# Optimization experiments

Measured on AMD Instinct MI355X. Metric: run time of the kernel, lower is better.

Reference implementation:

```python
import jax, jax.numpy as jnp
import numpy as np
from jax import lax

B, C, H, W = 4, 64, 256, 256
T, Q = 16, 0.2
C2 = 2 * C


def conv2d(x, w, b, pad):
    y = lax.conv_general_dilated(x, w, (1, 1), [(pad, pad), (pad, pad)],
                                 dimension_numbers=('NCHW', 'OIHW', 'NCHW'))
    return y + b[None, :, None, None]


def setup_inputs() -> dict:
    key = jax.random.key(0)
    ks = jax.random.split(key, 10)
    x = jax.random.normal(ks[0], (B, C, H, W), dtype=jnp.float32)
    lms = jax.random.normal(ks[1], (B, 4, H, W), dtype=jnp.float32)
    # params (kaiming-ish scale)
    W_conv = jax.random.normal(ks[2], (C2, C, 3, 3), dtype=jnp.float32) * (1.0 / np.sqrt(C * 9))
    b_conv = jnp.zeros((C2,), dtype=jnp.float32)
    W_out = jax.random.normal(ks[3], (4, C2), dtype=jnp.float32) * (1.0 / np.sqrt(C2))  # 1x1 conv as matrix
    b_out = jnp.zeros((4,), dtype=jnp.float32)
    W_aue = jax.random.normal(ks[4], (4, C2, 3, 3), dtype=jnp.float32) * (1.0 / np.sqrt(C2 * 9))
    b_aue = jnp.zeros((4,), dtype=jnp.float32)
    # T Bernoulli(1-q) channel masks, fixed for reproducibility  [T, 2C]
    masks = jax.random.bernoulli(ks[5], 1.0 - Q, (T, C2)).astype(jnp.float32)
    return {"x": x, "lms": lms, "W_conv": W_conv, "b_conv": b_conv,
            "W_out": W_out, "b_out": b_out, "W_aue": W_aue, "b_aue": b_aue,
            "masks": masks}


def reference(x, lms, W_conv, b_conv, W_out, b_out, W_aue, b_aue, masks):
    # feature extraction: 3x3 conv C -> 2C
    h = conv2d(x, W_conv, b_conv, 1)                      # [B, 2C, H, W]
    # MC-dropout samples: out(mask_t * h) == (W_out * mask_t) @ h  (1x1 conv is linear)
    Wt = W_out[None, :, :] * masks[:, None, :]            # [T, 4, 2C]
    samples = jnp.tanh(jnp.einsum('toc,bchw->tbohw', Wt, h)
                       + b_out[None, None, :, None, None]) + lms[None]  # [T, B, 4, H, W]
    mean = jnp.mean(samples, axis=0)
    EU = jnp.var(samples, axis=0, ddof=1)                 # unbiased variance over T
    AU = jax.nn.sigmoid(conv2d(h, W_aue, b_aue, 1))       # [B, 4, H, W]
    return (AU, EU, mean)
```

## Files before the change

kernel.cpp:

```cpp
#include <hip/hip_runtime.h>

#define Bsz 4
#define Cin 64
#define C2c 128
#define Hh 256
#define Ww 256
#define Tt 16
#define HW (Hh*Ww)
#define PLANE (Bsz*4*HW)

typedef __attribute__((ext_vector_type(8))) short bf16x8;
typedef __attribute__((ext_vector_type(4))) float f32x4;

#define XT_OFF  0
#define WBF_OFF 33554432
#define WTB_OFF 33701888
#define AUB_OFF 33718272

#define XP 76
#define HP 132

__device__ __forceinline__ unsigned short f2bf(float f) {
  union { float f; unsigned u; } cv; cv.f = f;
  unsigned u = cv.u;
  unsigned r = (u + 0x7fffu + ((u >> 16) & 1u)) >> 16;
  return (unsigned short)r;
}

union U8 { uint2 u2[2]; uint4 u4; bf16x8 v; };

__global__ void prep_kernel(const float* __restrict__ W_out, const float* __restrict__ masks,
                            const float* __restrict__ Wc, const float* __restrict__ W_aue,
                            unsigned short* __restrict__ Wtb, unsigned short* __restrict__ Wbf,
                            unsigned short* __restrict__ Aub) {
  int i = blockIdx.x * 256 + threadIdx.x;
  if (i < 8192) {
    int to = i >> 7, c = i & 127;
    int t = to >> 2, o = to & 3;
    Wtb[i] = f2bf(W_out[o * C2c + c] * masks[t * C2c + c]);
  } else if (i < 8192 + 73728) {
    int idx = i - 8192;
    int j = idx & 7;
    int lane = (idx >> 3) & 63;
    int nt = (idx >> 9) & 7;
    int c = idx >> 12;
    int q = lane >> 4;
    int tap = c >> 1;
    int ic = (c & 1) * 32 + q * 8 + j;
    int n = nt * 16 + (lane & 15);
    Wbf[idx] = f2bf(Wc[((size_t)n * Cin + ic) * 9 + tap]);
  } else if (i < 8192 + 73728 + 18432) {
    int idx = i - 8192 - 73728;
    int m = idx / 1152, k = idx % 1152;
    int tap = k >> 7, c = k & 127;
    float v = (m < 4) ? W_aue[((size_t)m * C2c + c) * 9 + tap] : 0.f;
    Aub[idx] = f2bf(v);
  }
}

__global__ __launch_bounds__(256) void xt_kernel(const float* __restrict__ x,
                                                 unsigned short* __restrict__ xT) {
  __shared__ unsigned short xs[64][65];
  const int tid = threadIdx.x;
  const int x0 = blockIdx.x * 64, y = blockIdx.y, bi = blockIdx.z;
  const int tx = tid & 63, ti = tid >> 6;
  #pragma unroll
  for (int i = 0; i < 16; ++i) {
    int ic = ti * 16 + i;
    float v = x[(((size_t)bi * Cin + ic) * Hh + y) * Ww + x0 + tx];
    xs[ic][tx] = f2bf(v);
  }
  __syncthreads();
  const int icg = tid & 7, xl = tid >> 3;
  #pragma unroll
  for (int rep = 0; rep < 2; ++rep) {
    int xx = xl + 32 * rep;
    unsigned short u[8];
    #pragma unroll
    for (int k = 0; k < 8; ++k) u[k] = xs[icg * 8 + k][xx];
    *(uint4*)(xT + (((size_t)bi * Hh + y) * Ww + (x0 + xx)) * Cin + icg * 8) = *(uint4*)u;
  }
}

__global__ __launch_bounds__(256, 3) void fused_kernel(
    const unsigned short* __restrict__ xT, const unsigned short* __restrict__ Wbf,
    const unsigned short* __restrict__ Wtb, const unsigned short* __restrict__ Aub,
    const float* __restrict__ bc, const float* __restrict__ b_out,
    const float* __restrict__ b_aue, const float* __restrict__ lms,
    float* __restrict__ out) {
  __shared__ unsigned short sh[192 * HP];
  const int tid = threadIdx.x;
  const int x0 = blockIdx.x * 16, y0 = blockIdx.y * 8, bi = blockIdx.z;

  for (int g = tid; g < 12 * 20 * 8; g += 256) {
    int icg = g & 7;
    int xc = (g >> 3) % 20;
    int xr = g / 160;
    int gy = y0 - 2 + xr, gx = x0 - 2 + xc;
    uint2 lo = make_uint2(0, 0), hi = make_uint2(0, 0);
    if ((unsigned)gy < Hh && (unsigned)gx < Ww) {
      uint4 v = *(const uint4*)(xT + (((size_t)bi * Hh + gy) * Ww + gx) * Cin + icg * 8);
      lo.x = v.x; lo.y = v.y; hi.x = v.z; hi.y = v.w;
    }
    int e = (xr * 20 + xc) * XP + icg * 8;
    *(uint2*)(&sh[e]) = lo;
    *(uint2*)(&sh[e + 4]) = hi;
  }
  __syncthreads();

  const int lane = tid & 63, wv = tid >> 6;
  const int n16 = lane & 15, q = lane >> 4;

  int xbase[3];
  #pragma unroll
  for (int s = 0; s < 3; ++s) {
    int px = (wv * 3 + s) * 16 + n16;
    int pr = px / 18, pc = px % 18;
    xbase[s] = (pr * 20 + pc) * XP + q * 8;
  }

  f32x4 acc[3][8];
  #pragma unroll
  for (int s = 0; s < 3; ++s)
    #pragma unroll
    for (int mt = 0; mt < 8; ++mt) acc[s][mt] = (f32x4){0.f, 0.f, 0.f, 0.f};

  #pragma unroll
  for (int c = 0; c < 18; ++c) {
    const int tap = c >> 1, ichalf = (c & 1) * 32;
    const int dy = tap / 3, dx = tap % 3;
    const int xoff = (dy * 20 + dx) * XP + ichalf;
    bf16x8 xfr[3];
    #pragma unroll
    for (int s = 0; s < 3; ++s) {
      U8 t;
      int e = xbase[s] + xoff;
      t.u2[0] = *(const uint2*)(&sh[e]);
      t.u2[1] = *(const uint2*)(&sh[e + 4]);
      xfr[s] = t.v;
    }
    #pragma unroll
    for (int mh = 0; mh < 2; ++mh) {
      bf16x8 wfr[4];
      const unsigned short* wb = Wbf + ((size_t)(c * 8 + mh * 4) * 64 + lane) * 8;
      #pragma unroll
      for (int i4 = 0; i4 < 4; ++i4)
        wfr[i4] = ((const U8*)(wb + i4 * 512))->v;
      #pragma unroll
      for (int s = 0; s < 3; ++s)
        #pragma unroll
        for (int i4 = 0; i4 < 4; ++i4)
          acc[s][mh * 4 + i4] =
            __builtin_amdgcn_mfma_f32_16x16x32_bf16(wfr[i4], xfr[s], acc[s][mh * 4 + i4], 0, 0, 0);
    }
  }
  __syncthreads();

  #pragma unroll
  for (int s = 0; s < 3; ++s) {
    const int px = (wv * 3 + s) * 16 + n16;
    const int pr = px / 18, pc = px % 18;
    const int gy = y0 - 1 + pr, gx = x0 - 1 + pc;
    const bool valid = ((unsigned)gy < Hh) && ((unsigned)gx < Ww);
    #pragma unroll
    for (int mt = 0; mt < 8; ++mt) {
      const int oc0 = mt * 16 + q * 4;
      const float4 b4 = *(const float4*)(bc + oc0);
      ushort4 o4;
      o4.x = valid ? f2bf(acc[s][mt][0] + b4.x) : (unsigned short)0;
      o4.y = valid ? f2bf(acc[s][mt][1] + b4.y) : (unsigned short)0;
      o4.z = valid ? f2bf(acc[s][mt][2] + b4.z) : (unsigned short)0;
      o4.w = valid ? f2bf(acc[s][mt][3] + b4.w) : (unsigned short)0;
      *(ushort4*)(&sh[px * HP + oc0]) = o4;
    }
  }
  __syncthreads();

  f32x4 accG[2][4];
  f32x4 accA[2];
  #pragma unroll
  for (int nt = 0; nt < 2; ++nt) {
    accA[nt] = (f32x4){0.f, 0.f, 0.f, 0.f};
    #pragma unroll
    for (int mt = 0; mt < 4; ++mt) accG[nt][mt] = (f32x4){0.f, 0.f, 0.f, 0.f};
  }

  #pragma unroll
  for (int kc = 0; kc < 4; ++kc) {
    bf16x8 afr[4];
    #pragma unroll
    for (int mt = 0; mt < 4; ++mt)
      afr[mt] = ((const U8*)(Wtb + (size_t)(mt * 16 + n16) * C2c + kc * 32 + q * 8))->v;
    #pragma unroll
    for (int nt = 0; nt < 2; ++nt) {
      int e = (((wv * 2 + nt) + 1) * 18 + n16 + 1) * HP + kc * 32 + q * 8;
      U8 b;
      b.u2[0] = *(const uint2*)(&sh[e]);
      b.u2[1] = *(const uint2*)(&sh[e + 4]);
      #pragma unroll
      for (int mt = 0; mt < 4; ++mt)
        accG[nt][mt] = __builtin_amdgcn_mfma_f32_16x16x32_bf16(afr[mt], b.v, accG[nt][mt], 0, 0, 0);
    }
  }

  #pragma unroll
  for (int kc = 0; kc < 36; ++kc) {
    const int tap = kc >> 2, co = (kc & 3) * 32;
    const int dy = tap / 3, dx = tap % 3;
    bf16x8 afr = ((const U8*)(Aub + (size_t)n16 * 1152 + kc * 32 + q * 8))->v;
    #pragma unroll
    for (int nt = 0; nt < 2; ++nt) {
      int e = ((wv * 2 + nt + dy) * 18 + n16 + dx) * HP + co + q * 8;
      U8 b;
      b.u2[0] = *(const uint2*)(&sh[e]);
      b.u2[1] = *(const uint2*)(&sh[e + 4]);
      accA[nt] = __builtin_amdgcn_mfma_f32_16x16x32_bf16(afr, b.v, accA[nt], 0, 0, 0);
    }
  }

  const float b0 = b_out[0], b1 = b_out[1], b2 = b_out[2], b3 = b_out[3];
  const float ba = b_aue[q];
  const int px = x0 + n16;
  #pragma unroll
  for (int nt = 0; nt < 2; ++nt) {
    const int y = y0 + wv * 2 + nt;
    float th[4][4];
    #pragma unroll
    for (int mt = 0; mt < 4; ++mt) {
      #pragma unroll
      for (int r = 0; r < 4; ++r) {
        float bo = (r == 0) ? b0 : (r == 1) ? b1 : (r == 2) ? b2 : b3;
        float v = accG[nt][mt][r] + bo;
        float e = __expf(2.f * v);
        th[mt][r] = 1.f - 2.f / (e + 1.f);
      }
    }
    float mean_r[4], eu_r[4];
    #pragma unroll
    for (int r = 0; r < 4; ++r) {
      float s = th[0][r] + th[1][r] + th[2][r] + th[3][r];
      s += __shfl_xor(s, 16);
      s += __shfl_xor(s, 32);
      float m = s * (1.f / 16.f);
      float d0 = th[0][r] - m, d1 = th[1][r] - m, d2 = th[2][r] - m, d3 = th[3][r] - m;
      float vs = d0 * d0 + d1 * d1 + d2 * d2 + d3 * d3;
      vs += __shfl_xor(vs, 16);
      vs += __shfl_xor(vs, 32);
      mean_r[r] = m;
      eu_r[r] = vs * (1.f / 15.f);
    }
    float au_r[4];
    #pragma unroll
    for (int r = 0; r < 4; ++r) au_r[r] = __shfl(accA[nt][r], n16);

    float m_q  = (q == 0) ? mean_r[0] : (q == 1) ? mean_r[1] : (q == 2) ? mean_r[2] : mean_r[3];
    float eu_q = (q == 0) ? eu_r[0]   : (q == 1) ? eu_r[1]   : (q == 2) ? eu_r[2]   : eu_r[3];
    float au_q = (q == 0) ? au_r[0]   : (q == 1) ? au_r[1]   : (q == 2) ? au_r[2]   : au_r[3];
    au_q = 1.f / (1.f + __expf(-(au_q + ba)));
    size_t oidx = ((size_t)(bi * 4 + q)) * HW + (size_t)y * Ww + px;
    float lm = lms[oidx];
    out[oidx] = au_q;
    out[PLANE + oidx] = eu_q;
    out[2 * (size_t)PLANE + oidx] = m_q + lm;
  }
}

extern "C" void kernel_launch(void* const* d_in, const int* in_sizes, int n_in,
                              void* d_out, int out_size, void* d_ws, size_t ws_size,
                              hipStream_t stream) {
  const float* x      = (const float*)d_in[0];
  const float* lms    = (const float*)d_in[1];
  const float* W_conv = (const float*)d_in[2];
  const float* b_conv = (const float*)d_in[3];
  const float* W_out  = (const float*)d_in[4];
  const float* b_out  = (const float*)d_in[5];
  const float* W_aue  = (const float*)d_in[6];
  const float* b_aue  = (const float*)d_in[7];
  const float* masks  = (const float*)d_in[8];
  float* out = (float*)d_out;

  char* ws = (char*)d_ws;
  unsigned short* xT  = (unsigned short*)(ws + XT_OFF);
  unsigned short* Wbf = (unsigned short*)(ws + WBF_OFF);
  unsigned short* Wtb = (unsigned short*)(ws + WTB_OFF);
  unsigned short* Aub = (unsigned short*)(ws + AUB_OFF);

  prep_kernel<<<dim3(392), dim3(256), 0, stream>>>(W_out, masks, W_conv, W_aue, Wtb, Wbf, Aub);
  xt_kernel<<<dim3(4, 256, 4), dim3(256), 0, stream>>>(x, xT);
  fused_kernel<<<dim3(16, 32, 4), dim3(256), 0, stream>>>(xT, Wbf, Wtb, Aub, b_conv,
                                                          b_out, b_aue, lms, out);
}
```

Baseline: 224.0 us.

## Merge prep into transpose kernel, async LDS loads with swizzled layouts

Folds the weight-prep kernel into the x-transpose kernel as an extra grid slice, which removes one launch, and widens the transpose to float4 loads with packed bf16 conversion. The fused kernel now fills its input halo tile with direct global-to-LDS loads (reading a zero pad buffer for out-of-range pixels), split into two channel halves so compute on the first half can start while the second half is still arriving. The padded LDS strides are replaced by XOR-swizzled layouts that allow single 16-byte LDS reads. The kernel also raises wave priority around MFMA bursts, skips stores for unused pixel slots, and shrinks the AU weight matrix to four rows. The explicit waitcnt and barrier ordering is fragile and must exactly match the number of loads issued.

Result: faster. 216.4 us (-3.4%).

```diff
diff --git a/kernel.cpp b/kernel.cpp
--- a/kernel.cpp
+++ b/kernel.cpp
@@ -16,9 +16,12 @@
 #define WBF_OFF 33554432
 #define WTB_OFF 33701888
 #define AUB_OFF 33718272
-
-#define XP 76
-#define HP 132
+#define ZP_OFF  33727488
+
+#define N_WTB 8192
+#define N_WBF 73728
+#define N_AUB 4608
+#define N_ZP  64
 
 __device__ __forceinline__ unsigned short f2bf(float f) {
   union { float f; unsigned u; } cv; cv.f = f;
@@ -27,96 +30,113 @@
   return (unsigned short)r;
 }
 
+__device__ __forceinline__ unsigned cvtpk(float a, float b) {
+  unsigned r;
+  asm("v_cvt_pk_bf16_f32 %0, %1, %2" : "=v"(r) : "v"(a), "v"(b));
+  return r;
+}
+
 union U8 { uint2 u2[2]; uint4 u4; bf16x8 v; };
 
-__global__ void prep_kernel(const float* __restrict__ W_out, const float* __restrict__ masks,
-                            const float* __restrict__ Wc, const float* __restrict__ W_aue,
-                            unsigned short* __restrict__ Wtb, unsigned short* __restrict__ Wbf,
-                            unsigned short* __restrict__ Aub) {
-  int i = blockIdx.x * 256 + threadIdx.x;
-  if (i < 8192) {
-    int to = i >> 7, c = i & 127;
-    int t = to >> 2, o = to & 3;
-    Wtb[i] = f2bf(W_out[o * C2c + c] * masks[t * C2c + c]);
-  } else if (i < 8192 + 73728) {
-    int idx = i - 8192;
-    int j = idx & 7;
-    int lane = (idx >> 3) & 63;
-    int nt = (idx >> 9) & 7;
-    int c = idx >> 12;
-    int q = lane >> 4;
-    int tap = c >> 1;
-    int ic = (c & 1) * 32 + q * 8 + j;
-    int n = nt * 16 + (lane & 15);
-    Wbf[idx] = f2bf(Wc[((size_t)n * Cin + ic) * 9 + tap]);
-  } else if (i < 8192 + 73728 + 18432) {
-    int idx = i - 8192 - 73728;
-    int m = idx / 1152, k = idx % 1152;
-    int tap = k >> 7, c = k & 127;
-    float v = (m < 4) ? W_aue[((size_t)m * C2c + c) * 9 + tap] : 0.f;
-    Aub[idx] = f2bf(v);
-  }
-}
-
-__global__ __launch_bounds__(256) void xt_kernel(const float* __restrict__ x,
-                                                 unsigned short* __restrict__ xT) {
-  __shared__ unsigned short xs[64][65];
+#define GLOAD16(g, l) __builtin_amdgcn_global_load_lds( \
+    (const __attribute__((address_space(1))) unsigned int*)(g), \
+    (__attribute__((address_space(3))) unsigned int*)(l), 16, 0, 0)
+
+__global__ __launch_bounds__(256) void xtp_kernel(
+    const float* __restrict__ x, const float* __restrict__ W_out,
+    const float* __restrict__ masks, const float* __restrict__ Wc,
+    const float* __restrict__ W_aue,
+    unsigned short* __restrict__ xT, unsigned short* __restrict__ Wtb,
+    unsigned short* __restrict__ Wbf, unsigned short* __restrict__ Aub,
+    unsigned short* __restrict__ Zp) {
+  __shared__ unsigned short xs[64 * 132];
   const int tid = threadIdx.x;
-  const int x0 = blockIdx.x * 64, y = blockIdx.y, bi = blockIdx.z;
-  const int tx = tid & 63, ti = tid >> 6;
-  #pragma unroll
-  for (int i = 0; i < 16; ++i) {
-    int ic = ti * 16 + i;
-    float v = x[(((size_t)bi * Cin + ic) * Hh + y) * Ww + x0 + tx];
-    xs[ic][tx] = f2bf(v);
+
+  if (blockIdx.z == 4) {
+    int i = (blockIdx.y * 2 + blockIdx.x) * 256 + tid;
+    if (i < N_WTB) {
+      int to = i >> 7, c = i & 127;
+      int t = to >> 2, o = to & 3;
+      Wtb[i] = f2bf(W_out[o * C2c + c] * masks[t * C2c + c]);
+    } else if (i < N_WTB + N_WBF) {
+      int idx = i - N_WTB;
+      int j = idx & 7;
+      int lane = (idx >> 3) & 63;
+      int nt = (idx >> 9) & 7;
+      int c = idx >> 12;
+      int qq = lane >> 4;
+      int tap = c >> 1;
+      int ic = (c & 1) * 32 + qq * 8 + j;
+      int n = nt * 16 + (lane & 15);
+      Wbf[idx] = f2bf(Wc[((size_t)n * Cin + ic) * 9 + tap]);
+    } else if (i < N_WTB + N_WBF + N_AUB) {
+      int idx = i - N_WTB - N_WBF;
+      int m = idx / 1152, k = idx % 1152;
+      int tap = k >> 7, c = k & 127;
+      Aub[idx] = f2bf(W_aue[((size_t)m * C2c + c) * 9 + tap]);
+    } else if (i < N_WTB + N_WBF + N_AUB + N_ZP) {
+      Zp[i - N_WTB - N_WBF - N_AUB] = 0;
+    }
+    return;
+  }
+
+  const int x0 = blockIdx.x * 128, y = blockIdx.y, bi = blockIdx.z;
+  #pragma unroll
+  for (int i = 0; i < 8; ++i) {
+    int idx = i * 256 + tid;
+    int ic = idx >> 5, xq = idx & 31;
+    float4 v = *(const float4*)(x + (((size_t)bi * Cin + ic) * Hh + y) * Ww + x0 + xq * 4);
+    *(uint2*)(&xs[ic * 132 + xq * 4]) = make_uint2(cvtpk(v.x, v.y), cvtpk(v.z, v.w));
   }
   __syncthreads();
-  const int icg = tid & 7, xl = tid >> 3;
-  #pragma unroll
-  for (int rep = 0; rep < 2; ++rep) {
-    int xx = xl + 32 * rep;
+  #pragma unroll
+  for (int j = 0; j < 4; ++j) {
+    int idx = j * 256 + tid;
+    int px = idx >> 3, icg = idx & 7;
     unsigned short u[8];
     #pragma unroll
-    for (int k = 0; k < 8; ++k) u[k] = xs[icg * 8 + k][xx];
-    *(uint4*)(xT + (((size_t)bi * Hh + y) * Ww + (x0 + xx)) * Cin + icg * 8) = *(uint4*)u;
+    for (int k = 0; k < 8; ++k) u[k] = xs[(icg * 8 + k) * 132 + px];
+    *(uint4*)(xT + (((size_t)bi * Hh + y) * Ww + (x0 + px)) * Cin + icg * 8) = *(uint4*)u;
   }
 }
 
 __global__ __launch_bounds__(256, 3) void fused_kernel(
     const unsigned short* __restrict__ xT, const unsigned short* __restrict__ Wbf,
     const unsigned short* __restrict__ Wtb, const unsigned short* __restrict__ Aub,
+    const unsigned short* __restrict__ Zp,
     const float* __restrict__ bc, const float* __restrict__ b_out,
     const float* __restrict__ b_aue, const float* __restrict__ lms,
     float* __restrict__ out) {
-  __shared__ unsigned short sh[192 * HP];
+  __shared__ __align__(16) unsigned short sh[23040];
   const int tid = threadIdx.x;
   const int x0 = blockIdx.x * 16, y0 = blockIdx.y * 8, bi = blockIdx.z;
 
-  for (int g = tid; g < 12 * 20 * 8; g += 256) {
-    int icg = g & 7;
-    int xc = (g >> 3) % 20;
-    int xr = g / 160;
-    int gy = y0 - 2 + xr, gx = x0 - 2 + xc;
-    uint2 lo = make_uint2(0, 0), hi = make_uint2(0, 0);
-    if ((unsigned)gy < Hh && (unsigned)gx < Ww) {
-      uint4 v = *(const uint4*)(xT + (((size_t)bi * Hh + gy) * Ww + gx) * Cin + icg * 8);
-      lo.x = v.x; lo.y = v.y; hi.x = v.z; hi.y = v.w;
-    }
-    int e = (xr * 20 + xc) * XP + icg * 8;
-    *(uint2*)(&sh[e]) = lo;
-    *(uint2*)(&sh[e + 4]) = hi;
-  }
-  __syncthreads();
+  #pragma unroll
+  for (int hf = 0; hf < 2; ++hf) {
+    #pragma unroll
+    for (int i = 0; i < 4; ++i) {
+      int g = i * 256 + tid;
+      int r = g >> 2;
+      int l = (g & 3) ^ (r & 3);
+      int pr = r / 20, pc = r - pr * 20;
+      int gy = y0 - 2 + pr, gx = x0 - 2 + pc;
+      bool ok = (r < 240) && ((unsigned)gy < Hh) && ((unsigned)gx < Ww);
+      const unsigned short* src = ok
+        ? xT + (((size_t)bi * Hh + gy) * Ww + gx) * Cin + (hf * 4 + l) * 8
+        : Zp;
+      GLOAD16(src, &sh[hf * 8192 + g * 8]);
+    }
+  }
 
   const int lane = tid & 63, wv = tid >> 6;
   const int n16 = lane & 15, q = lane >> 4;
 
-  int xbase[3];
+  int rbase[3];
   #pragma unroll
   for (int s = 0; s < 3; ++s) {
     int px = (wv * 3 + s) * 16 + n16;
     int pr = px / 18, pc = px % 18;
-    xbase[s] = (pr * 20 + pc) * XP + q * 8;
+    rbase[s] = pr * 20 + pc;
   }
 
   f32x4 acc[3][8];
@@ -125,33 +145,45 @@
     #pragma unroll
     for (int mt = 0; mt < 8; ++mt) acc[s][mt] = (f32x4){0.f, 0.f, 0.f, 0.f};
 
-  #pragma unroll
-  for (int c = 0; c < 18; ++c) {
-    const int tap = c >> 1, ichalf = (c & 1) * 32;
-    const int dy = tap / 3, dx = tap % 3;
-    const int xoff = (dy * 20 + dx) * XP + ichalf;
-    bf16x8 xfr[3];
-    #pragma unroll
-    for (int s = 0; s < 3; ++s) {
-      U8 t;
-      int e = xbase[s] + xoff;
-      t.u2[0] = *(const uint2*)(&sh[e]);
-      t.u2[1] = *(const uint2*)(&sh[e + 4]);
-      xfr[s] = t.v;
-    }
-    #pragma unroll
-    for (int mh = 0; mh < 2; ++mh) {
-      bf16x8 wfr[4];
-      const unsigned short* wb = Wbf + ((size_t)(c * 8 + mh * 4) * 64 + lane) * 8;
-      #pragma unroll
-      for (int i4 = 0; i4 < 4; ++i4)
-        wfr[i4] = ((const U8*)(wb + i4 * 512))->v;
-      #pragma unroll
-      for (int s = 0; s < 3; ++s)
+  asm volatile("s_waitcnt vmcnt(4)" ::: "memory");
+  __builtin_amdgcn_s_barrier();
+  __builtin_amdgcn_sched_barrier(0);
+
+  #pragma unroll
+  for (int hf = 0; hf < 2; ++hf) {
+    if (hf == 1) {
+      asm volatile("s_waitcnt vmcnt(0)" ::: "memory");
+      __builtin_amdgcn_s_barrier();
+      __builtin_amdgcn_sched_barrier(0);
+    }
+    #pragma unroll
+    for (int tap = 0; tap < 9; ++tap) {
+      const int dd = (tap / 3) * 20 + (tap % 3);
+      const int c = tap * 2 + hf;
+      bf16x8 xfr[3];
+      #pragma unroll
+      for (int s = 0; s < 3; ++s) {
+        int rr = rbase[s] + dd;
+        int a = hf * 8192 + rr * 32 + ((q ^ (rr & 3)) << 3);
+        U8 t; t.u4 = *(const uint4*)(&sh[a]);
+        xfr[s] = t.v;
+      }
+      #pragma unroll
+      for (int mh = 0; mh < 2; ++mh) {
+        bf16x8 wfr[4];
+        const unsigned short* wb = Wbf + ((size_t)(c * 8 + mh * 4) * 64 + lane) * 8;
         #pragma unroll
         for (int i4 = 0; i4 < 4; ++i4)
-          acc[s][mh * 4 + i4] =
-            __builtin_amdgcn_mfma_f32_16x16x32_bf16(wfr[i4], xfr[s], acc[s][mh * 4 + i4], 0, 0, 0);
+          wfr[i4] = ((const U8*)(wb + i4 * 512))->v;
+        __builtin_amdgcn_s_setprio(1);
+        #pragma unroll
+        for (int s = 0; s < 3; ++s)
+          #pragma unroll
+          for (int i4 = 0; i4 < 4; ++i4)
+            acc[s][mh * 4 + i4] =
+              __builtin_amdgcn_mfma_f32_16x16x32_bf16(wfr[i4], xfr[s], acc[s][mh * 4 + i4], 0, 0, 0);
+        __builtin_amdgcn_s_setprio(0);
+      }
     }
   }
   __syncthreads();
@@ -159,19 +191,21 @@
   #pragma unroll
   for (int s = 0; s < 3; ++s) {
     const int px = (wv * 3 + s) * 16 + n16;
-    const int pr = px / 18, pc = px % 18;
-    const int gy = y0 - 1 + pr, gx = x0 - 1 + pc;
-    const bool valid = ((unsigned)gy < Hh) && ((unsigned)gx < Ww);
-    #pragma unroll
-    for (int mt = 0; mt < 8; ++mt) {
-      const int oc0 = mt * 16 + q * 4;
-      const float4 b4 = *(const float4*)(bc + oc0);
-      ushort4 o4;
-      o4.x = valid ? f2bf(acc[s][mt][0] + b4.x) : (unsigned short)0;
-      o4.y = valid ? f2bf(acc[s][mt][1] + b4.y) : (unsigned short)0;
-      o4.z = valid ? f2bf(acc[s][mt][2] + b4.z) : (unsigned short)0;
-      o4.w = valid ? f2bf(acc[s][mt][3] + b4.w) : (unsigned short)0;
-      *(ushort4*)(&sh[px * HP + oc0]) = o4;
+    if (px < 180) {
+      const int pr = px / 18, pc = px % 18;
+      const int gy = y0 - 1 + pr, gx = x0 - 1 + pc;
+      const bool valid = ((unsigned)gy < Hh) && ((unsigned)gx < Ww);
+      const int key = px & 15;
+      #pragma unroll
+      for (int mt = 0; mt < 8; ++mt) {
+        const int oc0 = mt * 16 + q * 4;
+        const float4 b4 = *(const float4*)(bc + oc0);
+        unsigned lo = cvtpk(acc[s][mt][0] + b4.x, acc[s][mt][1] + b4.y);
+        unsigned hi = cvtpk(acc[s][mt][2] + b4.z, acc[s][mt][3] + b4.w);
+        if (!valid) { lo = 0u; hi = 0u; }
+        int a = px * 128 + (((mt * 2 + (q >> 1)) ^ key) << 3) + (q & 1) * 4;
+        *(uint2*)(&sh[a]) = make_uint2(lo, hi);
+      }
     }
   }
   __syncthreads();
@@ -193,10 +227,9 @@
       afr[mt] = ((const U8*)(Wtb + (size_t)(mt * 16 + n16) * C2c + kc * 32 + q * 8))->v;
     #pragma unroll
     for (int nt = 0; nt < 2; ++nt) {
-      int e = (((wv * 2 + nt) + 1) * 18 + n16 + 1) * HP + kc * 32 + q * 8;
-      U8 b;
-      b.u2[0] = *(const uint2*)(&sh[e]);
-      b.u2[1] = *(const uint2*)(&sh[e + 4]);
+      int hr = (wv * 2 + nt + 1) * 18 + n16 + 1;
+      int a = hr * 128 + (((kc * 4 + q) ^ (hr & 15)) << 3);
+      U8 b; b.u4 = *(const uint4*)(&sh[a]);
       #pragma unroll
       for (int mt = 0; mt < 4; ++mt)
         accG[nt][mt] = __builtin_amdgcn_mfma_f32_16x16x32_bf16(afr[mt], b.v, accG[nt][mt], 0, 0, 0);
@@ -205,15 +238,14 @@
 
   #pragma unroll
   for (int kc = 0; kc < 36; ++kc) {
-    const int tap = kc >> 2, co = (kc & 3) * 32;
+    const int tap = kc >> 2, co4 = kc & 3;
     const int dy = tap / 3, dx = tap % 3;
-    bf16x8 afr = ((const U8*)(Aub + (size_t)n16 * 1152 + kc * 32 + q * 8))->v;
+    bf16x8 afr = ((const U8*)(Aub + (size_t)(n16 & 3) * 1152 + kc * 32 + q * 8))->v;
     #pragma unroll
     for (int nt = 0; nt < 2; ++nt) {
-      int e = ((wv * 2 + nt + dy) * 18 + n16 + dx) * HP + co + q * 8;
-      U8 b;
-      b.u2[0] = *(const uint2*)(&sh[e]);
-      b.u2[1] = *(const uint2*)(&sh[e + 4]);
+      int hr = (wv * 2 + nt + dy) * 18 + n16 + dx;
+      int a = hr * 128 + (((co4 * 4 + q) ^ (hr & 15)) << 3);
+      U8 b; b.u4 = *(const uint4*)(&sh[a]);
       accA[nt] = __builtin_amdgcn_mfma_f32_16x16x32_bf16(afr, b.v, accA[nt], 0, 0, 0);
     }
   }
@@ -284,9 +316,10 @@
   unsigned short* Wbf = (unsigned short*)(ws + WBF_OFF);
   unsigned short* Wtb = (unsigned short*)(ws + WTB_OFF);
   unsigned short* Aub = (unsigned short*)(ws + AUB_OFF);
-
-  prep_kernel<<<dim3(392), dim3(256), 0, stream>>>(W_out, masks, W_conv, W_aue, Wtb, Wbf, Aub);
-  xt_kernel<<<dim3(4, 256, 4), dim3(256), 0, stream>>>(x, xT);
-  fused_kernel<<<dim3(16, 32, 4), dim3(256), 0, stream>>>(xT, Wbf, Wtb, Aub, b_conv,
+  unsigned short* Zp  = (unsigned short*)(ws + ZP_OFF);
+
+  xtp_kernel<<<dim3(2, 256, 5), dim3(256), 0, stream>>>(x, W_out, masks, W_conv, W_aue,
+                                                        xT, Wtb, Wbf, Aub, Zp);
+  fused_kernel<<<dim3(16, 32, 4), dim3(256), 0, stream>>>(xT, Wbf, Wtb, Aub, Zp, b_conv,
                                                           b_out, b_aue, lms, out);
 }
```
